# Kernel optimization log

Hardware: AMD Instinct MI355X
Metric: run time of the kernel (lower is better)

The kernel has to match this reference:

```python
import jax, jax.numpy as jnp
import numpy as np
import math

B, S, HID, H = 8, 512, 768, 12
D = HID // H  # 64
LABEL_VOCAB = 2 * 40 + 1  # 81
EPS = 1e-5


def layernorm(x, g, b):
    mu = jnp.mean(x, axis=-1, keepdims=True)
    var = jnp.var(x, axis=-1, keepdims=True)
    return (x - mu) * jax.lax.rsqrt(var + EPS) * g + b


def setup_inputs() -> dict:
    key = jax.random.key(0)
    ks = jax.random.split(key, 12)
    s = 0.02
    return {
        "hidden_states": jax.random.normal(ks[0], (B, S, HID), jnp.float32),
        "attention_mask": jnp.zeros((B, 1, 1, S), jnp.float32),
        "graph_arc": jax.random.randint(ks[1], (B, S, S), 0, LABEL_VOCAB, jnp.int32),
        "Wq": jax.random.normal(ks[2], (HID, HID), jnp.float32) * s,
        "bq": jnp.zeros((HID,), jnp.float32),
        "Wk": jax.random.normal(ks[3], (HID, HID), jnp.float32) * s,
        "bk": jnp.zeros((HID,), jnp.float32),
        "Wv": jax.random.normal(ks[4], (HID, HID), jnp.float32) * s,
        "bv": jnp.zeros((HID,), jnp.float32),
        "rel_k": jax.random.normal(ks[5], (LABEL_VOCAB, D), jnp.float32) * s,
        "rel_v": jax.random.normal(ks[6], (LABEL_VOCAB, D), jnp.float32) * s,
        "ln_k_g": jnp.ones((D,), jnp.float32),
        "ln_k_b": jnp.zeros((D,), jnp.float32),
        "ln_v_g": jnp.ones((D,), jnp.float32),
        "ln_v_b": jnp.zeros((D,), jnp.float32),
    }


def reference(hidden_states, attention_mask, graph_arc, Wq, bq, Wk, bk, Wv, bv,
              rel_k, rel_v, ln_k_g, ln_k_b, ln_v_g, ln_v_b):
    # projections -> [B, H, S, D]
    def split_heads(x):
        return x.reshape(B, S, H, D).transpose(0, 2, 1, 3)

    q = split_heads(hidden_states @ Wq + bq)
    k = split_heads(hidden_states @ Wk + bk)
    v = split_heads(hidden_states @ Wv + bv)

    # relation embeddings [B, S, S, D], layernormed over D
    dp_keys = layernorm(rel_k[graph_arc], ln_k_g, ln_k_b)
    dp_values = layernorm(rel_v[graph_arc], ln_v_g, ln_v_b)

    scores = jnp.einsum('bhqd,bhkd->bhqk', q, k) / math.sqrt(D)
    # relative_matmul_dp: per (b, q-position) GEMM of q[B,S,H,D] with dp_keys^T
    scores = scores + jnp.einsum('bqhd,bqkd->bhqk', q.transpose(0, 2, 1, 3), dp_keys)
    scores = scores + attention_mask

    probs = jax.nn.softmax(scores, axis=-1)  # dropout p=0 (eval)

    ctx = jnp.einsum('bhqk,bhkd->bqhd', probs, v)
    # relative_matmul_dpv
    ctx = ctx + jnp.einsum('bhqk,bqkd->bqhd', probs, dp_values)
    return ctx.reshape(B, S, HID)
```

## Files before the change

kernel.cpp:

```cpp
#include <hip/hip_runtime.h>
#include <hip/hip_bf16.h>

#define BB 8
#define SS 512
#define HIDV 768
#define HH 12
#define DD 64
#define LV 81

typedef __attribute__((ext_vector_type(8))) short short8v;
typedef __attribute__((ext_vector_type(4))) short short4v;
typedef __attribute__((ext_vector_type(4))) float f32x4;

#define MFMA16(a, b, c) __builtin_amdgcn_mfma_f32_16x16x32_bf16(a, b, c, 0, 0, 0)

__device__ __forceinline__ short f2bf(float f) {
    __hip_bfloat16 h = __float2bfloat16(f);
    return *reinterpret_cast<short*>(&h);
}
__device__ __forceinline__ void gload16(const void* g, void* l) {
    __builtin_amdgcn_global_load_lds((const __attribute__((address_space(1))) void*)g,
                                     (__attribute__((address_space(3))) void*)l, 16, 0, 0);
}

__global__ __launch_bounds__(256) void prep_ln_kernel(
    const float* __restrict__ rel_k, const float* __restrict__ rel_v,
    const float* __restrict__ gk, const float* __restrict__ bk,
    const float* __restrict__ gv, const float* __restrict__ bv,
    short* __restrict__ lnkb, short* __restrict__ lnvT) {
    __shared__ float ln_lds[2 * LV][DD];
    int t = threadIdx.x;
    if (t < 2 * LV) {
        bool isv = (t >= LV);
        int r = isv ? t - LV : t;
        const float* row = (isv ? rel_v : rel_k) + r * DD;
        const float* g = isv ? gv : gk;
        const float* be = isv ? bv : bk;
        float mu = 0.f;
        for (int d = 0; d < DD; ++d) mu += row[d];
        mu *= (1.f / DD);
        float var = 0.f;
        for (int d = 0; d < DD; ++d) { float x = row[d] - mu; var += x * x; }
        var *= (1.f / DD);
        float rs = rsqrtf(var + 1e-5f);
        for (int d = 0; d < DD; ++d) ln_lds[t][d] = (row[d] - mu) * rs * g[d] + be[d];
    }
    __syncthreads();
    for (int i = t; i < 96 * DD; i += 256) {
        int l = i >> 6, d = i & 63;
        lnkb[i] = (l < LV) ? f2bf(ln_lds[l][d]) : (short)0;
    }
    for (int i = t; i < DD * 96; i += 256) {
        int d = i / 96, ll = i - d * 96;
        lnvT[i] = (ll < LV) ? f2bf(ln_lds[LV + ll][d]) : (short)0;
    }
}

__global__ __launch_bounds__(256) void conv_hidden_kernel(const float* __restrict__ in,
                                                          short* __restrict__ out) {
    int i = (blockIdx.x * 256 + threadIdx.x) * 4;
    float4 v = *reinterpret_cast<const float4*>(&in[i]);
    short4v o; o[0] = f2bf(v.x); o[1] = f2bf(v.y); o[2] = f2bf(v.z); o[3] = f2bf(v.w);
    *reinterpret_cast<short4v*>(&out[i]) = o;
}

__global__ __launch_bounds__(256) void transw_kernel(
    const float* __restrict__ Wq, const float* __restrict__ Wk, const float* __restrict__ Wv,
    short* __restrict__ WqT, short* __restrict__ WkT, short* __restrict__ WvT) {
    const float* W; short* O;
    if (blockIdx.z == 0) { W = Wq; O = WqT; }
    else if (blockIdx.z == 1) { W = Wk; O = WkT; }
    else { W = Wv; O = WvT; }
    __shared__ float tile[32][33];
    int k0 = blockIdx.y * 32, n0 = blockIdx.x * 32;
    int t = threadIdx.x;
    int r = t >> 3, c4 = (t & 7) * 4;
    float4 v = *reinterpret_cast<const float4*>(&W[(size_t)(k0 + r) * HIDV + n0 + c4]);
    tile[r][c4 + 0] = v.x; tile[r][c4 + 1] = v.y; tile[r][c4 + 2] = v.z; tile[r][c4 + 3] = v.w;
    __syncthreads();
    short4v o;
    o[0] = f2bf(tile[c4 + 0][r]); o[1] = f2bf(tile[c4 + 1][r]);
    o[2] = f2bf(tile[c4 + 2][r]); o[3] = f2bf(tile[c4 + 3][r]);
    *reinterpret_cast<short4v*>(&O[(size_t)(n0 + r) * HIDV + k0 + c4]) = o;
}

__global__ __launch_bounds__(256) void arcpack_kernel(const int* __restrict__ arc,
                                                      unsigned int* __restrict__ arcP) {
    __shared__ unsigned int tbuf[64][129];
    const int tid = threadIdx.x;
    const int b = blockIdx.y;
    const int q0 = blockIdx.x * 64;
    for (int i = tid; i < 64 * 128; i += 256) {
        int r = i >> 7, c4 = i & 127;
        int4 v = *reinterpret_cast<const int4*>(&arc[((size_t)(b * SS) + q0 + r) * SS + 4 * c4]);
        tbuf[r][c4] = (unsigned)(v.x & 255) | ((unsigned)(v.y & 255) << 8) |
                      ((unsigned)(v.z & 255) << 16) | ((unsigned)(v.w & 255) << 24);
    }
    __syncthreads();
    for (int i = tid; i < 128 * 64; i += 256) {
        int k4 = i >> 6, r = i & 63;
        arcP[((size_t)b * 128 + k4) * SS + q0 + r] = tbuf[r][k4];
    }
}

__global__ __launch_bounds__(256) void qkv_gemm_kernel(
    const short* __restrict__ Abf,
    const short* __restrict__ WqT, const short* __restrict__ WkT, const short* __restrict__ WvT,
    const float* __restrict__ bq, const float* __restrict__ bk, const float* __restrict__ bv,
    short* __restrict__ qo, short* __restrict__ ko, short* __restrict__ vto) {
    const short* Bt; const float* bias;
    int z = blockIdx.z;
    if (z == 0) { Bt = WqT; bias = bq; }
    else if (z == 1) { Bt = WkT; bias = bk; }
    else { Bt = WvT; bias = bv; }

    __shared__ short smem[8192];
    short* As = smem;
    short* Bs = smem + 4096;

    const int tid = threadIdx.x;
    const int lane = tid & 63, w = tid >> 6;
    const int li = lane & 15, g = lane >> 4;
    const int wr = w >> 1, wc = w & 1;
    const int m0 = blockIdx.y * 64, n0 = blockIdx.x * 64;

    f32x4 acc[2][2];
    for (int ra = 0; ra < 2; ++ra)
        for (int cb = 0; cb < 2; ++cb)
            for (int r = 0; r < 4; ++r) acc[ra][cb][r] = 0.f;

#pragma unroll 1
    for (int k0 = 0; k0 < HIDV; k0 += 64) {
#pragma unroll
        for (int j = 0; j < 2; ++j) {
            int c = j * 256 + tid;
            int row = c >> 3, s = c & 7;
            int src = s ^ (row & 7);
            gload16(Abf + (size_t)(m0 + row) * HIDV + k0 + src * 8, As + c * 8);
            gload16(Bt + (size_t)(n0 + row) * HIDV + k0 + src * 8, Bs + c * 8);
        }
        __syncthreads();
#pragma unroll
        for (int c = 0; c < 2; ++c) {
            short8v af[2], bf[2];
#pragma unroll
            for (int ra = 0; ra < 2; ++ra) {
                int row = 32 * wr + 16 * ra + li;
                int chunk = (4 * c + g) ^ (row & 7);
                af[ra] = *reinterpret_cast<const short8v*>(&As[row * 64 + chunk * 8]);
            }
#pragma unroll
            for (int cb = 0; cb < 2; ++cb) {
                int rowb = 32 * wc + 16 * cb + li;
                int chunk = (4 * c + g) ^ (rowb & 7);
                bf[cb] = *reinterpret_cast<const short8v*>(&Bs[rowb * 64 + chunk * 8]);
            }
#pragma unroll
            for (int ra = 0; ra < 2; ++ra)
#pragma unroll
                for (int cb = 0; cb < 2; ++cb)
                    acc[ra][cb] = MFMA16(af[ra], bf[cb], acc[ra][cb]);
        }
        __syncthreads();
    }

    const int h = n0 >> 6;
    const int bidx = m0 >> 9;
    if (z < 2) {
        short* dst = (z == 0) ? qo : ko;
        float sc = (z == 0) ? 1.f : 0.125f;
#pragma unroll
        for (int ra = 0; ra < 2; ++ra)
#pragma unroll
            for (int cb = 0; cb < 2; ++cb) {
                int n = 32 * wc + 16 * cb + li;
                float bv_ = bias[n0 + n];
#pragma unroll
                for (int r = 0; r < 4; ++r) {
                    int m = m0 + 32 * wr + 16 * ra + 4 * g + r;
                    int s = m & 511;
                    dst[(((size_t)bidx * HH + h) * SS + s) * DD + n] =
                        f2bf((acc[ra][cb][r] + bv_) * sc);
                }
            }
    } else {
        short* Cs = smem;
#pragma unroll
        for (int ra = 0; ra < 2; ++ra)
#pragma unroll
            for (int cb = 0; cb < 2; ++cb) {
                int nl = 32 * wc + 16 * cb + li;
                float bv_ = bias[n0 + nl];
#pragma unroll
                for (int r = 0; r < 4; ++r) {
                    int ml = 32 * wr + 16 * ra + 4 * g + r;
                    Cs[nl * 72 + ml] = f2bf(acc[ra][cb][r] + bv_);
                }
            }
        __syncthreads();
        for (int c = tid; c < 512; c += 256) {
            int dl = c >> 3, s8 = (c & 7) * 8;
            short8v vv = *reinterpret_cast<const short8v*>(&Cs[dl * 72 + s8]);
            *reinterpret_cast<short8v*>(
                &vto[(((size_t)bidx * HH + h) * DD + dl) * SS + (m0 & 511) + s8]) = vv;
        }
    }
}

__global__ __launch_bounds__(256, 2) void attn_kernel(
    const short* __restrict__ qb, const short* __restrict__ kb, const short* __restrict__ vt,
    const unsigned int* __restrict__ arcP, const float* __restrict__ maskp,
    const short* __restrict__ lnkb, const short* __restrict__ lnvT,
    float* __restrict__ outp) {
    __shared__ float qlds[4][16][84];
    __shared__ float bucket[4][16][100];

    const int tid = threadIdx.x;
    const int w = tid >> 6, lane = tid & 63;
    const int li = lane & 15, g = lane >> 4;
    const int bx = blockIdx.x;
    const int b = bx & 7;
    const int rest = bx >> 3;
    const int h = rest % HH, qt = rest / HH;
    const int bh = b * HH + h;
    const int q0 = qt * 64 + w * 16;

    const short* kbp = kb + (size_t)bh * SS * DD;
    const short* vbp = vt + (size_t)bh * DD * SS;
    const unsigned int* apb = arcP + (size_t)b * 128 * SS;
    const float* mkb = maskp + (size_t)b * SS;

    for (int i = lane; i < 16 * 100; i += 64) (&bucket[w][0][0])[i] = 0.f;

    short8v qf0, qf1;
    {
        const short* qrow = qb + ((size_t)bh * SS + q0 + li) * DD + 8 * g;
        qf0 = *reinterpret_cast<const short8v*>(qrow);
        qf1 = *reinterpret_cast<const short8v*>(qrow + 32);
    }

#pragma unroll
    for (int ct = 0; ct < 6; ++ct) {
        f32x4 a = {0.f, 0.f, 0.f, 0.f};
        short8v b0 = *reinterpret_cast<const short8v*>(&lnkb[(16 * ct + li) * DD + 8 * g]);
        short8v b1 = *reinterpret_cast<const short8v*>(&lnkb[(16 * ct + li) * DD + 32 + 8 * g]);
        a = MFMA16(qf0, b0, a);
        a = MFMA16(qf1, b1, a);
        if (16 * ct + li < 84)
#pragma unroll
            for (int r = 0; r < 4; ++r) qlds[w][4 * g + r][16 * ct + li] = a[r];
    }

    f32x4 oacc[4];
    for (int t = 0; t < 4; ++t) for (int r = 0; r < 4; ++r) oacc[t][r] = 0.f;

    short8v kf[8];
    unsigned int a_[2][4];
    float4 m_[2][4];
#pragma unroll
    for (int t = 0; t < 4; ++t) {
        const short* kr = kbp + (size_t)(16 * t + li) * DD + 8 * g;
        kf[2 * t] = *reinterpret_cast<const short8v*>(kr);
        kf[2 * t + 1] = *reinterpret_cast<const short8v*>(kr + 32);
        a_[0][t] = apb[(size_t)(4 * t + g) * SS + q0 + li];
        m_[0][t] = *reinterpret_cast<const float4*>(&mkb[16 * t + 4 * g]);
    }

#pragma unroll
    for (int kt = 0; kt < 8; ++kt) {
        const int cur = kt & 1, nxt = cur ^ 1;
        const int kb0 = kt * 64;

        f32x4 sacc[4];
#pragma unroll
        for (int t = 0; t < 4; ++t) {
            f32x4 a = {0.f, 0.f, 0.f, 0.f};
            a = MFMA16(kf[2 * t], qf0, a);
            a = MFMA16(kf[2 * t + 1], qf1, a);
            sacc[t] = a;
        }

        if (kt < 7) {
#pragma unroll
            for (int t = 0; t < 4; ++t) {
                const short* kr = kbp + (size_t)(kb0 + 64 + 16 * t + li) * DD + 8 * g;
                kf[2 * t] = *reinterpret_cast<const short8v*>(kr);
                kf[2 * t + 1] = *reinterpret_cast<const short8v*>(kr + 32);
                a_[nxt][t] = apb[(size_t)((kt + 1) * 16 + 4 * t + g) * SS + q0 + li];
                m_[nxt][t] = *reinterpret_cast<const float4*>(&mkb[kb0 + 64 + 16 * t + 4 * g]);
            }
        }

        float p[16];
#pragma unroll
        for (int t = 0; t < 4; ++t) {
            const unsigned int a4 = a_[cur][t];
            float qv0 = qlds[w][li][a4 & 255];
            float qv1 = qlds[w][li][(a4 >> 8) & 255];
            float qv2 = qlds[w][li][(a4 >> 16) & 255];
            float qv3 = qlds[w][li][a4 >> 24];
            p[4 * t + 0] = __expf(sacc[t][0] + qv0 + m_[cur][t].x);
            p[4 * t + 1] = __expf(sacc[t][1] + qv1 + m_[cur][t].y);
            p[4 * t + 2] = __expf(sacc[t][2] + qv2 + m_[cur][t].z);
            p[4 * t + 3] = __expf(sacc[t][3] + qv3 + m_[cur][t].w);
        }

#pragma unroll
        for (int t = 0; t < 4; ++t) {
            const unsigned int a4 = a_[cur][t];
            unsafeAtomicAdd(&bucket[w][li][a4 & 255], p[4 * t + 0]);
            unsafeAtomicAdd(&bucket[w][li][(a4 >> 8) & 255], p[4 * t + 1]);
            unsafeAtomicAdd(&bucket[w][li][(a4 >> 16) & 255], p[4 * t + 2]);
            unsafeAtomicAdd(&bucket[w][li][a4 >> 24], p[4 * t + 3]);
        }

        short8v pfrag[2];
#pragma unroll
        for (int t = 0; t < 4; ++t)
#pragma unroll
            for (int r = 0; r < 4; ++r) pfrag[t >> 1][4 * (t & 1) + r] = f2bf(p[4 * t + r]);
#pragma unroll
        for (int dt = 0; dt < 2; ++dt) {
#pragma unroll
            for (int t2 = 0; t2 < 4; ++t2) {
                const short* vr = vbp + (size_t)(16 * t2 + li) * SS + kb0 + 32 * dt + 4 * g;
                short4v v0 = *reinterpret_cast<const short4v*>(vr);
                short4v v1 = *reinterpret_cast<const short4v*>(vr + 16);
                short8v vf;
                vf[0] = v0[0]; vf[1] = v0[1]; vf[2] = v0[2]; vf[3] = v0[3];
                vf[4] = v1[0]; vf[5] = v1[1]; vf[6] = v1[2]; vf[7] = v1[3];
                oacc[t2] = MFMA16(pfrag[dt], vf, oacc[t2]);
            }
        }
    }

    float lsum = 0.f;
#pragma unroll
    for (int j = 0; j < 24; ++j) {
        int c = 24 * g + j;
        lsum += (c < 81) ? bucket[w][li][c] : 0.f;
    }
    lsum += __shfl_xor(lsum, 16);
    lsum += __shfl_xor(lsum, 32);
    float inv = 1.f / lsum;
    float invr[4];
#pragma unroll
    for (int r = 0; r < 4; ++r) invr[r] = __shfl(inv, 4 * g + r);

    f32x4 racc[4];
    for (int t = 0; t < 4; ++t) for (int r = 0; r < 4; ++r) racc[t][r] = 0.f;
#pragma unroll
    for (int c = 0; c < 3; ++c) {
        f32x4 b0 = *reinterpret_cast<const f32x4*>(&bucket[w][li][8 * g + 32 * c]);
        f32x4 b1 = *reinterpret_cast<const f32x4*>(&bucket[w][li][8 * g + 32 * c + 4]);
        short8v bfr;
        bfr[0] = f2bf(b0[0]); bfr[1] = f2bf(b0[1]); bfr[2] = f2bf(b0[2]); bfr[3] = f2bf(b0[3]);
        bfr[4] = f2bf(b1[0]); bfr[5] = f2bf(b1[1]); bfr[6] = f2bf(b1[2]); bfr[7] = f2bf(b1[3]);
#pragma unroll
        for (int t2 = 0; t2 < 4; ++t2) {
            short8v lf = *reinterpret_cast<const short8v*>(
                &lnvT[(16 * t2 + li) * 96 + 8 * g + 32 * c]);
            racc[t2] = MFMA16(bfr, lf, racc[t2]);
        }
    }

#pragma unroll
    for (int t2 = 0; t2 < 4; ++t2)
#pragma unroll
        for (int r = 0; r < 4; ++r) {
            int row = q0 + 4 * g + r;
            outp[((size_t)b * SS + row) * HIDV + h * DD + 16 * t2 + li] =
                (oacc[t2][r] + racc[t2][r]) * invr[r];
        }
}

extern "C" void kernel_launch(void* const* d_in, const int* in_sizes, int n_in,
                              void* d_out, int out_size, void* d_ws, size_t ws_size,
                              hipStream_t stream) {
    const float* hidden = (const float*)d_in[0];
    const float* mask   = (const float*)d_in[1];
    const int*   arc    = (const int*)d_in[2];
    const float* Wq = (const float*)d_in[3];
    const float* bq = (const float*)d_in[4];
    const float* Wk = (const float*)d_in[5];
    const float* bk = (const float*)d_in[6];
    const float* Wv = (const float*)d_in[7];
    const float* bv = (const float*)d_in[8];
    const float* rel_k = (const float*)d_in[9];
    const float* rel_v = (const float*)d_in[10];
    const float* lng_k = (const float*)d_in[11];
    const float* lnb_k = (const float*)d_in[12];
    const float* lng_v = (const float*)d_in[13];
    const float* lnb_v = (const float*)d_in[14];
    float* out = (float*)d_out;

    char* p = (char*)d_ws;
    auto carve = [&](size_t bytes) { char* r = p; p += (bytes + 255) & ~(size_t)255; return r; };
    short* lnkb = (short*)carve((size_t)96 * DD * 2);
    short* lnvT = (short*)carve((size_t)DD * 96 * 2);
    short* hbf  = (short*)carve((size_t)BB * SS * HIDV * 2);
    short* WqT  = (short*)carve((size_t)HIDV * HIDV * 2);
    short* WkT  = (short*)carve((size_t)HIDV * HIDV * 2);
    short* WvT  = (short*)carve((size_t)HIDV * HIDV * 2);
    const size_t per = (size_t)BB * HH * SS * DD;
    short* qbuf = (short*)carve(per * 2);
    short* kbuf = (short*)carve(per * 2);
    short* vtb  = (short*)carve(per * 2);
    unsigned int* arcP = (unsigned int*)carve((size_t)BB * 128 * SS * 4);

    prep_ln_kernel<<<1, 256, 0, stream>>>(rel_k, rel_v, lng_k, lnb_k, lng_v, lnb_v, lnkb, lnvT);
    conv_hidden_kernel<<<(BB * SS * HIDV) / 1024, 256, 0, stream>>>(hidden, hbf);
    transw_kernel<<<dim3(24, 24, 3), 256, 0, stream>>>(Wq, Wk, Wv, WqT, WkT, WvT);
    arcpack_kernel<<<dim3(8, BB), 256, 0, stream>>>(arc, arcP);
    qkv_gemm_kernel<<<dim3(HIDV / 64, (BB * SS) / 64, 3), 256, 0, stream>>>(
        hbf, WqT, WkT, WvT, bq, bk, bv, qbuf, kbuf, vtb);
    attn_kernel<<<dim3(BB * HH * 8), 256, 0, stream>>>(
        qbuf, kbuf, vtb, arcP, mask, lnkb, lnvT, out);
}
```

Before: 196.0 us.

## Enlarge QKV GEMM tile to 128x128 and store relation-key scores as fp16

```diff
diff --git a/kernel.cpp b/kernel.cpp
--- a/kernel.cpp
+++ b/kernel.cpp
@@ -17,6 +17,12 @@
 __device__ __forceinline__ short f2bf(float f) {
     __hip_bfloat16 h = __float2bfloat16(f);
     return *reinterpret_cast<short*>(&h);
+}
+__device__ __forceinline__ short f2h(float f) {
+    _Float16 h = (_Float16)f; short s; __builtin_memcpy(&s, &h, 2); return s;
+}
+__device__ __forceinline__ float h2f(short s) {
+    _Float16 h; __builtin_memcpy(&h, &s, 2); return (float)h;
 }
 __device__ __forceinline__ void gload16(const void* g, void* l) {
     __builtin_amdgcn_global_load_lds((const __attribute__((address_space(1))) void*)g,
@@ -114,25 +120,27 @@
     else if (z == 1) { Bt = WkT; bias = bk; }
     else { Bt = WvT; bias = bv; }
 
-    __shared__ short smem[8192];
+    __shared__ short smem[17408];
     short* As = smem;
-    short* Bs = smem + 4096;
+    short* Bs = smem + 8192;
 
     const int tid = threadIdx.x;
     const int lane = tid & 63, w = tid >> 6;
     const int li = lane & 15, g = lane >> 4;
     const int wr = w >> 1, wc = w & 1;
-    const int m0 = blockIdx.y * 64, n0 = blockIdx.x * 64;
-
-    f32x4 acc[2][2];
-    for (int ra = 0; ra < 2; ++ra)
-        for (int cb = 0; cb < 2; ++cb)
+    const int m0 = blockIdx.y * 128, n0 = blockIdx.x * 128;
+
+    f32x4 acc[4][4];
+#pragma unroll
+    for (int ra = 0; ra < 4; ++ra)
+#pragma unroll
+        for (int cb = 0; cb < 4; ++cb)
             for (int r = 0; r < 4; ++r) acc[ra][cb][r] = 0.f;
 
 #pragma unroll 1
     for (int k0 = 0; k0 < HIDV; k0 += 64) {
 #pragma unroll
-        for (int j = 0; j < 2; ++j) {
+        for (int j = 0; j < 4; ++j) {
             int c = j * 256 + tid;
             int row = c >> 3, s = c & 7;
             int src = s ^ (row & 7);
@@ -142,65 +150,69 @@
         __syncthreads();
 #pragma unroll
         for (int c = 0; c < 2; ++c) {
-            short8v af[2], bf[2];
-#pragma unroll
-            for (int ra = 0; ra < 2; ++ra) {
-                int row = 32 * wr + 16 * ra + li;
+            short8v af[4], bf[4];
+#pragma unroll
+            for (int ra = 0; ra < 4; ++ra) {
+                int row = 64 * wr + 16 * ra + li;
                 int chunk = (4 * c + g) ^ (row & 7);
                 af[ra] = *reinterpret_cast<const short8v*>(&As[row * 64 + chunk * 8]);
             }
 #pragma unroll
-            for (int cb = 0; cb < 2; ++cb) {
-                int rowb = 32 * wc + 16 * cb + li;
+            for (int cb = 0; cb < 4; ++cb) {
+                int rowb = 64 * wc + 16 * cb + li;
                 int chunk = (4 * c + g) ^ (rowb & 7);
                 bf[cb] = *reinterpret_cast<const short8v*>(&Bs[rowb * 64 + chunk * 8]);
             }
 #pragma unroll
-            for (int ra = 0; ra < 2; ++ra)
-#pragma unroll
-                for (int cb = 0; cb < 2; ++cb)
+            for (int ra = 0; ra < 4; ++ra)
+#pragma unroll
+                for (int cb = 0; cb < 4; ++cb)
                     acc[ra][cb] = MFMA16(af[ra], bf[cb], acc[ra][cb]);
         }
         __syncthreads();
     }
 
-    const int h = n0 >> 6;
     const int bidx = m0 >> 9;
     if (z < 2) {
         short* dst = (z == 0) ? qo : ko;
         float sc = (z == 0) ? 1.f : 0.125f;
 #pragma unroll
-        for (int ra = 0; ra < 2; ++ra)
-#pragma unroll
-            for (int cb = 0; cb < 2; ++cb) {
-                int n = 32 * wc + 16 * cb + li;
-                float bv_ = bias[n0 + n];
+        for (int ra = 0; ra < 4; ++ra)
+#pragma unroll
+            for (int cb = 0; cb < 4; ++cb) {
+                int n = n0 + 64 * wc + 16 * cb + li;
+                int h = n >> 6, d = n & 63;
+                float bv_ = bias[n];
 #pragma unroll
                 for (int r = 0; r < 4; ++r) {
-                    int m = m0 + 32 * wr + 16 * ra + 4 * g + r;
+                    int m = m0 + 64 * wr + 16 * ra + 4 * g + r;
                     int s = m & 511;
-                    dst[(((size_t)bidx * HH + h) * SS + s) * DD + n] =
+                    dst[(((size_t)bidx * HH + h) * SS + s) * DD + d] =
                         f2bf((acc[ra][cb][r] + bv_) * sc);
                 }
             }
     } else {
         short* Cs = smem;
 #pragma unroll
-        for (int ra = 0; ra < 2; ++ra)
-#pragma unroll
-            for (int cb = 0; cb < 2; ++cb) {
-                int nl = 32 * wc + 16 * cb + li;
+        for (int ra = 0; ra < 4; ++ra)
+#pragma unroll
+            for (int cb = 0; cb < 4; ++cb) {
+                int nl = 64 * wc + 16 * cb + li;
                 float bv_ = bias[n0 + nl];
 #pragma unroll
                 for (int r = 0; r < 4; ++r) {
-                    int ml = 32 * wr + 16 * ra + 4 * g + r;
-                    Cs[nl * 72 + ml] = f2bf(acc[ra][cb][r] + bv_);
+                    int ml = 64 * wr + 16 * ra + 4 * g + r;
+                    Cs[nl * 136 + ml] = f2bf(acc[ra][cb][r] + bv_);
                 }
             }
         __syncthreads();
-        for (int c = tid; c < 512; c += 256) {
-            int dl = c >> 3, s8 = (c & 7) * 8;
-            short8v vv = *reinterpret_cast<const short8v*>(&Cs[dl * 72 + s8]);
+        const int h0 = n0 >> 6;
+#pragma unroll
+        for (int j = 0; j < 8; ++j) {
+            int c = tid + 256 * j;
+            int col = c >> 4, s8 = (c & 15) * 8;
+            short8v vv = *reinterpret_cast<const short8v*>(&Cs[col * 136 + s8]);
+            int h = h0 + (col >> 6), dl = col & 63;
             *reinterpret_cast<short8v*>(
                 &vto[(((size_t)bidx * HH + h) * DD + dl) * SS + (m0 & 511) + s8]) = vv;
         }
@@ -212,7 +224,7 @@
     const unsigned int* __restrict__ arcP, const float* __restrict__ maskp,
     const short* __restrict__ lnkb, const short* __restrict__ lnvT,
     float* __restrict__ outp) {
-    __shared__ float qlds[4][16][84];
+    __shared__ short qlds[4][16][84];
     __shared__ float bucket[4][16][100];
 
     const int tid = threadIdx.x;
@@ -248,7 +260,7 @@
         a = MFMA16(qf1, b1, a);
         if (16 * ct + li < 84)
 #pragma unroll
-            for (int r = 0; r < 4; ++r) qlds[w][4 * g + r][16 * ct + li] = a[r];
+            for (int r = 0; r < 4; ++r) qlds[w][4 * g + r][16 * ct + li] = f2h(a[r]);
     }
 
     f32x4 oacc[4];
@@ -295,10 +307,10 @@
 #pragma unroll
         for (int t = 0; t < 4; ++t) {
             const unsigned int a4 = a_[cur][t];
-            float qv0 = qlds[w][li][a4 & 255];
-            float qv1 = qlds[w][li][(a4 >> 8) & 255];
-            float qv2 = qlds[w][li][(a4 >> 16) & 255];
-            float qv3 = qlds[w][li][a4 >> 24];
+            float qv0 = h2f(qlds[w][li][a4 & 255]);
+            float qv1 = h2f(qlds[w][li][(a4 >> 8) & 255]);
+            float qv2 = h2f(qlds[w][li][(a4 >> 16) & 255]);
+            float qv3 = h2f(qlds[w][li][a4 >> 24]);
             p[4 * t + 0] = __expf(sacc[t][0] + qv0 + m_[cur][t].x);
             p[4 * t + 1] = __expf(sacc[t][1] + qv1 + m_[cur][t].y);
             p[4 * t + 2] = __expf(sacc[t][2] + qv2 + m_[cur][t].z);
@@ -412,7 +424,7 @@
     conv_hidden_kernel<<<(BB * SS * HIDV) / 1024, 256, 0, stream>>>(hidden, hbf);
     transw_kernel<<<dim3(24, 24, 3), 256, 0, stream>>>(Wq, Wk, Wv, WqT, WkT, WvT);
     arcpack_kernel<<<dim3(8, BB), 256, 0, stream>>>(arc, arcP);
-    qkv_gemm_kernel<<<dim3(HIDV / 64, (BB * SS) / 64, 3), 256, 0, stream>>>(
+    qkv_gemm_kernel<<<dim3(HIDV / 128, (BB * SS) / 128, 3), 256, 0, stream>>>(
         hbf, WqT, WkT, WvT, bq, bk, bv, qbuf, kbuf, vtb);
     attn_kernel<<<dim3(BB * HH * 8), 256, 0, stream>>>(
         qbuf, kbuf, vtb, arcP, mask, lnkb, lnvT, out);
```

Result: slower. 202.8 us (+3.5%).
